# Kernel tuning notes

Measured on AMD Instinct MI355X. Metric: run time of the kernel, lower is better.

The kernel has to match this reference:

```python
import jax, jax.numpy as jnp
import numpy as np

N = 20000      # nodes
E = 320000     # edges
F_IN = 64      # input_dim
HID = 128      # hidden_dim
H = 2          # heads (hard-coded in BGA)
G = 64         # num graphs (batch_step_dim[0])
MID = 32       # middle_dim
OUT = 1        # output_dim
EPS = 1e-5


def setup_inputs() -> dict:
    key = jax.random.key(0)
    ks = jax.random.split(key, 24)
    p = lambda k, shape: jax.random.normal(k, shape, jnp.float32) * 0.05
    inp = {}
    inp["x"] = jax.random.normal(ks[0], (N, F_IN), jnp.float32)
    inp["edge_index"] = jax.random.randint(ks[1], (2, E), 0, N)
    inp["atten_edge_index"] = jax.random.randint(ks[2], (2, E), 0, N)
    inp["batch_index"] = jnp.sort(jax.random.randint(ks[3], (N,), 0, G))
    # GANConv 0 MLP (2-layer: Linear->BN->ReLU->Linear)
    inp["g0_w1"] = p(ks[4], (F_IN, HID)); inp["g0_b1"] = jnp.zeros((HID,), jnp.float32)
    inp["g0_bn_g"] = jnp.ones((HID,), jnp.float32); inp["g0_bn_b"] = jnp.zeros((HID,), jnp.float32)
    inp["g0_w2"] = p(ks[5], (HID, HID)); inp["g0_b2"] = jnp.zeros((HID,), jnp.float32)
    # GANConv 1 MLP
    inp["g1_w1"] = p(ks[6], (HID, HID)); inp["g1_b1"] = jnp.zeros((HID,), jnp.float32)
    inp["g1_bn_g"] = jnp.ones((HID,), jnp.float32); inp["g1_bn_b"] = jnp.zeros((HID,), jnp.float32)
    inp["g1_w2"] = p(ks[7], (HID, HID)); inp["g1_b2"] = jnp.zeros((HID,), jnp.float32)
    # BGA batch norms after each GANConv
    inp["bn0_g"] = jnp.ones((HID,), jnp.float32); inp["bn0_b"] = jnp.zeros((HID,), jnp.float32)
    inp["bn1_g"] = jnp.ones((HID,), jnp.float32); inp["bn1_b"] = jnp.zeros((HID,), jnp.float32)
    # ATTConv atten_self: in=HID, out=HID, heads=2, concat=True
    inp["a1_wl"] = p(ks[8], (HID, H * HID)); inp["a1_bl"] = jnp.zeros((H * HID,), jnp.float32)
    inp["a1_wr"] = p(ks[9], (HID, H * HID)); inp["a1_br"] = jnp.zeros((H * HID,), jnp.float32)
    inp["a1_att"] = p(ks[10], (H, HID))
    inp["a1_bias"] = jnp.zeros((H * HID,), jnp.float32)
    # ATTConv atten: in=H*HID, out=HID, heads=2, concat=False (mean over heads)
    inp["a2_wl"] = p(ks[11], (H * HID, H * HID)); inp["a2_bl"] = jnp.zeros((H * HID,), jnp.float32)
    inp["a2_wr"] = p(ks[12], (H * HID, H * HID)); inp["a2_br"] = jnp.zeros((H * HID,), jnp.float32)
    inp["a2_att"] = p(ks[13], (H, HID))
    inp["a2_bias"] = jnp.zeros((HID,), jnp.float32)
    # prediction heads (only layer 0 and last are used)
    inp["pred0_w"] = p(ks[14], (F_IN, MID)); inp["pred0_b"] = jnp.zeros((MID,), jnp.float32)
    inp["predL_w"] = p(ks[15], (HID, MID)); inp["predL_b"] = jnp.zeros((MID,), jnp.float32)
    inp["out_w"] = p(ks[16], (MID, OUT)); inp["out_b"] = jnp.zeros((OUT,), jnp.float32)
    return inp


def _bn(x, g, b):  # training-mode batch norm over node axis
    m = x.mean(0)
    v = x.var(0)
    return (x - m) * jax.lax.rsqrt(v + EPS) * g + b


def _mlp2(x, w1, b1, bn_g, bn_b, w2, b2):
    h = jax.nn.relu(_bn(x @ w1 + b1, bn_g, bn_b))
    return h @ w2 + b2


def _gan_conv(x, edge_index, w1, b1, bn_g, bn_b, w2, b2):
    row, col = edge_index[0], edge_index[1]
    agg = jax.ops.segment_sum(x[col], row, num_segments=x.shape[0])
    return _mlp2(x + agg, w1, b1, bn_g, bn_b, w2, b2)


def _att_conv(x, edge_index, wl, bl, wr, br, att, bias, concat):
    # GATv2-style: e = leaky_relu(x_i + x_j); alpha = softmax_dst(<e, att>)
    n = x.shape[0]
    xl = (x @ wl + bl).reshape(n, H, HID)  # source proj
    xr = (x @ wr + br).reshape(n, H, HID)  # target proj
    src, dst = edge_index[0], edge_index[1]
    e = jax.nn.leaky_relu(xl[src] + xr[dst], 0.2)          # [E,H,C]
    logit = jnp.einsum('ehc,hc->eh', e, att)               # [E,H]
    lmax = jax.ops.segment_max(logit, dst, num_segments=n)
    w = jnp.exp(logit - lmax[dst])
    denom = jax.ops.segment_sum(w, dst, num_segments=n)
    alpha = w / (denom[dst] + 1e-16)                       # [E,H]
    out = jax.ops.segment_sum(xl[src] * alpha[:, :, None], dst, num_segments=n)
    if concat:
        out = out.reshape(n, H * HID)
    else:
        out = out.mean(1)
    return out + bias, alpha


def reference(x, edge_index, atten_edge_index, batch_index,
              g0_w1, g0_b1, g0_bn_g, g0_bn_b, g0_w2, g0_b2,
              g1_w1, g1_b1, g1_bn_g, g1_bn_b, g1_w2, g1_b2,
              bn0_g, bn0_b, bn1_g, bn1_b,
              a1_wl, a1_bl, a1_wr, a1_br, a1_att, a1_bias,
              a2_wl, a2_bl, a2_wr, a2_br, a2_att, a2_bias,
              pred0_w, pred0_b, predL_w, predL_b, out_w, out_b):
    h0 = x
    h1 = jax.nn.relu(_bn(_gan_conv(h0, edge_index, g0_w1, g0_b1, g0_bn_g, g0_bn_b, g0_w2, g0_b2), bn0_g, bn0_b))
    h2 = jax.nn.relu(_bn(_gan_conv(h1, edge_index, g1_w1, g1_b1, g1_bn_g, g1_bn_b, g1_w2, g1_b2), bn1_g, bn1_b))
    emb, _ = _att_conv(h2, edge_index, a1_wl, a1_bl, a1_wr, a1_br, a1_att, a1_bias, concat=True)
    emb = jax.nn.relu(emb)
    atten_out, alpha = _att_conv(emb, atten_edge_index, a2_wl, a2_bl, a2_wr, a2_br, a2_att, a2_bias, concat=False)
    atten_out = jax.nn.relu(atten_out)
    pool0 = jax.ops.segment_sum(h0, batch_index, num_segments=G)
    poolL = jax.ops.segment_sum(atten_out, batch_index, num_segments=G)
    out_h = jax.nn.relu((pool0 @ pred0_w + pred0_b) + (poolL @ predL_w + predL_b))
    outputs = out_h @ out_w + out_b
    return (outputs, atten_out, alpha)
```

## Files before the change

kernel.cpp:

```cpp
#include <hip/hip_runtime.h>
#include <hip/hip_bf16.h>

#define N_NODES 20000
#define E_EDGES 320000
#define F_INN   64
#define HID     128
#define HEADS   2
#define HC      (HEADS * HID)
#define G_GR    64
#define MIDD    32
#define EPSV    1e-5f
#define NBUK    79

#define CDIV(a, b) (((a) + (b) - 1) / (b))

typedef __attribute__((ext_vector_type(8))) short          bf16x8;
typedef __attribute__((ext_vector_type(4))) float          f32x4;
typedef __attribute__((ext_vector_type(8))) unsigned short u16x8;

__device__ inline float bf2f(unsigned short u) { return __uint_as_float((unsigned)u << 16); }
__device__ inline unsigned short f2bf(float f) {
    unsigned u = __float_as_uint(f);
    unsigned r = u + 0x7FFFu + ((u >> 16) & 1u);
    return (unsigned short)(r >> 16);
}

#if __has_builtin(__builtin_amdgcn_exp2f)
__device__ inline float fexp2(float x) { return __builtin_amdgcn_exp2f(x); }
#else
__device__ inline float fexp2(float x) { return exp2f(x); }
#endif

struct Csr3 {
    const int* key[3];
    const int* other[3];
    int* btot;
    int* bstart;
    int* bcur;
    int* rowptr[3];
    int* out[3];
    int2* tmp;
};

__global__ __launch_bounds__(256) void k_bhist(Csr3 c) {
    __shared__ int hist[NBUK];
    const int y = blockIdx.y;
    const int chunk0 = blockIdx.x * 4096;
    const int t = threadIdx.x;
    for (int i = t; i < NBUK; i += 256) hist[i] = 0;
    __syncthreads();
#pragma unroll
    for (int i = 0; i < 16; i++) {
        int e = chunk0 + (i << 8) + t;
        if (e < E_EDGES) atomicAdd(&hist[c.key[y][e] >> 8], 1);
    }
    __syncthreads();
    for (int i = t; i < NBUK; i += 256)
        if (hist[i] > 0) atomicAdd(&c.btot[y * NBUK + i], hist[i]);
}

__global__ void k_bscan(Csr3 c) {
    __shared__ int sh[3 * NBUK];
    int t = threadIdx.x;
    for (int i = t; i < 3 * NBUK; i += 256) sh[i] = c.btot[i];
    __syncthreads();
    if (t < 3) {
        int run = 0;
        int* bs = c.bstart + t * (NBUK + 1);
        for (int b = 0; b < NBUK; b++) {
            bs[b] = run;
            c.bcur[t * NBUK + b] = run;
            run += sh[t * NBUK + b];
        }
        bs[NBUK] = run;
    }
}

__global__ __launch_bounds__(256) void k_bucketA(Csr3 c) {
    __shared__ int hist[NBUK], base[NBUK], off[NBUK];
    const int y = blockIdx.y;
    const int chunk0 = blockIdx.x * 4096;
    const int t = threadIdx.x;
    for (int i = t; i < NBUK; i += 256) { hist[i] = 0; off[i] = 0; }
    __syncthreads();
    int keys[16], vals[16], bks[16];
#pragma unroll
    for (int i = 0; i < 16; i++) {
        int e = chunk0 + (i << 8) + t;
        bool ok = (e < E_EDGES);
        int k = ok ? c.key[y][e] : 0;
        keys[i] = k;
        vals[i] = ok ? ((y == 2) ? e : c.other[y][e]) : 0;
        bks[i] = ok ? (k >> 8) : -1;
        if (ok) atomicAdd(&hist[k >> 8], 1);
    }
    __syncthreads();
    if (t < NBUK && hist[t] > 0) base[t] = atomicAdd(&c.bcur[y * NBUK + t], hist[t]);
    __syncthreads();
    int2* ty = c.tmp + (size_t)y * E_EDGES;
#pragma unroll
    for (int i = 0; i < 16; i++) {
        int b = bks[i];
        if (b >= 0) {
            int o = atomicAdd(&off[b], 1);
            ty[base[b] + o] = make_int2(keys[i], vals[i]);
        }
    }
}

__global__ __launch_bounds__(256) void k_bucketB(Csr3 c) {
    __shared__ int cnt[256], lbase[256], run[256];
    const int y = blockIdx.y;
    const int b = blockIdx.x;
    const int nbase = b << 8;
    const int t = threadIdx.x;
    cnt[t] = 0; run[t] = 0;
    __syncthreads();
    const int bs = c.bstart[y * (NBUK + 1) + b];
    const int be = c.bstart[y * (NBUK + 1) + b + 1];
    const int2* ty = c.tmp + (size_t)y * E_EDGES;
    for (int i = bs + t; i < be; i += 256)
        atomicAdd(&cnt[ty[i].x - nbase], 1);
    __syncthreads();
    int v = cnt[t];
    lbase[t] = v;
    __syncthreads();
    for (int off = 1; off < 256; off <<= 1) {
        int u = (t >= off) ? lbase[t - off] : 0;
        __syncthreads();
        lbase[t] += u;
        __syncthreads();
    }
    int excl = lbase[t] - v;
    __syncthreads();
    lbase[t] = excl;
    __syncthreads();
    int n = nbase + t;
    if (n < N_NODES) c.rowptr[y][n] = bs + excl;
    if (b == NBUK - 1 && t == 0) c.rowptr[y][N_NODES] = E_EDGES;
    int* outy = c.out[y];
    for (int i = bs + t; i < be; i += 256) {
        int2 kv = ty[i];
        int k = kv.x - nbase;
        int o = atomicAdd(&run[k], 1);
        outy[bs + lbase[k] + o] = kv.y;
    }
}

__global__ __launch_bounds__(256) void k_src_gather(const int* __restrict__ eids,
                                                    const int* __restrict__ srcs,
                                                    int* __restrict__ outv) {
    int i = blockIdx.x * 256 + threadIdx.x;
    if (i < E_EDGES) outv[i] = srcs[eids[i]];
}

__global__ __launch_bounds__(256) void k_gather_f32(const float4* __restrict__ x,
                                                    const int* __restrict__ rowptr,
                                                    const int* __restrict__ srcs,
                                                    unsigned short* __restrict__ z) {
    int gid = blockIdx.x * blockDim.x + threadIdx.x;
    int n = gid >> 4;
    if (n >= N_NODES) return;
    int q = gid & 15;
    float4 acc = x[((size_t)n << 4) + q];
    float4 a1 = make_float4(0.f, 0.f, 0.f, 0.f), a2 = a1, a3 = a1;
    int p = rowptr[n], p1 = rowptr[n + 1];
    for (; p + 4 <= p1; p += 4) {
        float4 v0 = x[((size_t)srcs[p + 0] << 4) + q];
        float4 v1 = x[((size_t)srcs[p + 1] << 4) + q];
        float4 v2 = x[((size_t)srcs[p + 2] << 4) + q];
        float4 v3 = x[((size_t)srcs[p + 3] << 4) + q];
        acc.x += v0.x; acc.y += v0.y; acc.z += v0.z; acc.w += v0.w;
        a1.x += v1.x; a1.y += v1.y; a1.z += v1.z; a1.w += v1.w;
        a2.x += v2.x; a2.y += v2.y; a2.z += v2.z; a2.w += v2.w;
        a3.x += v3.x; a3.y += v3.y; a3.z += v3.z; a3.w += v3.w;
    }
    for (; p < p1; p++) {
        float4 v = x[((size_t)srcs[p] << 4) + q];
        acc.x += v.x; acc.y += v.y; acc.z += v.z; acc.w += v.w;
    }
    acc.x += a1.x + a2.x + a3.x; acc.y += a1.y + a2.y + a3.y;
    acc.z += a1.z + a2.z + a3.z; acc.w += a1.w + a2.w + a3.w;
    ushort4 o;
    o.x = f2bf(acc.x); o.y = f2bf(acc.y); o.z = f2bf(acc.z); o.w = f2bf(acc.w);
    *(ushort4*)&z[((size_t)n << 6) + (q << 2)] = o;
}

__global__ __launch_bounds__(256) void k_gather_bn(const u16x8* __restrict__ raw,
                                                   const int* __restrict__ rowptr,
                                                   const int* __restrict__ srcs,
                                                   const float* __restrict__ bn_sums,
                                                   const float* __restrict__ g,
                                                   const float* __restrict__ b,
                                                   u16x8* __restrict__ z) {
    int gid = blockIdx.x * blockDim.x + threadIdx.x;
    int n = gid >> 4;
    if (n >= N_NODES) return;
    int q = gid & 15;
    float sc[8], sh[8];
#pragma unroll
    for (int i = 0; i < 8; i++) {
        int c = (q << 3) + i;
        float mean = bn_sums[c] / N_NODES;
        float istd = rsqrtf(bn_sums[HID + c] / N_NODES - mean * mean + EPSV);
        float s = istd * g[c];
        sc[i] = s;
        sh[i] = b[c] - mean * s;
    }
    u16x8 u0 = raw[((size_t)n << 4) + q];
    float acc[8];
#pragma unroll
    for (int i = 0; i < 8; i++) acc[i] = fmaxf(bf2f(u0[i]) * sc[i] + sh[i], 0.f);
    int p = rowptr[n], p1 = rowptr[n + 1];
    for (; p + 4 <= p1; p += 4) {
        u16x8 v0 = raw[((size_t)srcs[p + 0] << 4) + q];
        u16x8 v1 = raw[((size_t)srcs[p + 1] << 4) + q];
        u16x8 v2 = raw[((size_t)srcs[p + 2] << 4) + q];
        u16x8 v3 = raw[((size_t)srcs[p + 3] << 4) + q];
#pragma unroll
        for (int i = 0; i < 8; i++) {
            acc[i] += fmaxf(bf2f(v0[i]) * sc[i] + sh[i], 0.f)
                    + fmaxf(bf2f(v1[i]) * sc[i] + sh[i], 0.f)
                    + fmaxf(bf2f(v2[i]) * sc[i] + sh[i], 0.f)
                    + fmaxf(bf2f(v3[i]) * sc[i] + sh[i], 0.f);
        }
    }
    for (; p < p1; p++) {
        u16x8 v = raw[((size_t)srcs[p] << 4) + q];
#pragma unroll
        for (int i = 0; i < 8; i++) acc[i] += fmaxf(bf2f(v[i]) * sc[i] + sh[i], 0.f);
    }
    u16x8 o;
#pragma unroll
    for (int i = 0; i < 8; i++) o[i] = f2bf(acc[i]);
    z[((size_t)n << 4) + q] = o;
}

struct WtJob  { const float* src; unsigned short* dst; int K; int N; };
struct WtJobs { WtJob j[8]; };
__global__ void k_wt_cast(WtJobs jobs) {
    WtJob jb = jobs.j[blockIdx.y];
    int total = jb.K * jb.N;
    for (int i = blockIdx.x * blockDim.x + threadIdx.x; i < total; i += gridDim.x * blockDim.x) {
        int nn = i / jb.K, kk = i - nn * jb.K;
        jb.dst[i] = f2bf(jb.src[(size_t)kk * jb.N + nn]);
    }
}

template <int STATS, int BNA, int TM, int BIAS2>
__global__ __launch_bounds__(256) void k_mfma_gemm(const unsigned short* __restrict__ A,
                                                   const unsigned short* __restrict__ Wt,
                                                   const float* __restrict__ biasL,
                                                   const float* __restrict__ biasR,
                                                   unsigned short* __restrict__ Cout,
                                                   int M, int K, int N,
                                                   float* __restrict__ stats_sums,
                                                   const float* __restrict__ bn_sums,
                                                   const float* __restrict__ bn_g,
                                                   const float* __restrict__ bn_b) {
    constexpr int BNF = (TM == 128) ? 4 : 2;
    __shared__ unsigned short As[TM][40];
    __shared__ unsigned short Bs[128][40];
    __shared__ float s_scale[BNA ? HID : 1], s_shift[BNA ? HID : 1];
    const int t = threadIdx.x;
    if (BNA) {
        if (t < HID) {
            float mean = bn_sums[t] / M;
            float istd = rsqrtf(bn_sums[HID + t] / M - mean * mean + EPSV);
            float s = istd * bn_g[t];
            s_scale[t] = s;
            s_shift[t] = bn_b[t] - mean * s;
        }
        __syncthreads();
    }
    const int wave = t >> 6, lane = t & 63;
    const int row0 = blockIdx.y * TM, col0 = blockIdx.x * 128;
    const int wm = (TM == 128) ? ((wave & 1) << 6) : 0;
    const int wn = (TM == 128) ? ((wave >> 1) << 6) : (wave << 5);
    const int lm = lane & 15, lk = (lane >> 4) << 3;
    constexpr int APASS = TM / 64;
    f32x4 acc[4][BNF] = {};
    for (int k0 = 0; k0 < K; k0 += 32) {
        u16x8 av[APASS], wv[2];
#pragma unroll
        for (int i = 0; i < APASS; i++) {
            int c = t + (i << 8);
            int r = c >> 2, ko = (c & 3) << 3;
            u16x8 zv = {};
            int gr = row0 + r;
            av[i] = (gr < M) ? *(const u16x8*)&A[(size_t)gr * K + k0 + ko] : zv;
            if (BNA) {
#pragma unroll
                for (int j = 0; j < 8; j++) {
                    int kc = k0 + ko + j;
                    float v = fmaxf(bf2f(av[i][j]) * s_scale[kc] + s_shift[kc], 0.f);
                    av[i][j] = f2bf(v);
                }
            }
        }
#pragma unroll
        for (int i = 0; i < 2; i++) {
            int c = t + (i << 8);
            int r = c >> 2, ko = (c & 3) << 3;
            wv[i] = *(const u16x8*)&Wt[(size_t)(col0 + r) * K + k0 + ko];
        }
        __syncthreads();
#pragma unroll
        for (int i = 0; i < APASS; i++) {
            int c = t + (i << 8);
            int r = c >> 2, ko = (c & 3) << 3;
            *(u16x8*)&As[r][ko] = av[i];
        }
#pragma unroll
        for (int i = 0; i < 2; i++) {
            int c = t + (i << 8);
            int r = c >> 2, ko = (c & 3) << 3;
            *(u16x8*)&Bs[r][ko] = wv[i];
        }
        __syncthreads();
        bf16x8 af[4], bfm[BNF];
#pragma unroll
        for (int i = 0; i < 4; i++) af[i]  = *(const bf16x8*)&As[wm + (i << 4) + lm][lk];
#pragma unroll
        for (int j = 0; j < BNF; j++) bfm[j] = *(const bf16x8*)&Bs[wn + (j << 4) + lm][lk];
#pragma unroll
        for (int i = 0; i < 4; i++)
#pragma unroll
            for (int j = 0; j < BNF; j++)
                acc[i][j] = __builtin_amdgcn_mfma_f32_16x16x32_bf16(af[i], bfm[j], acc[i][j], 0, 0, 0);
    }
    const int lr4 = (lane >> 4) << 2;
    float s1[BNF], s2[BNF];
#pragma unroll
    for (int j = 0; j < BNF; j++) { s1[j] = 0.f; s2[j] = 0.f; }
#pragma unroll
    for (int j = 0; j < BNF; j++) {
        int col = col0 + wn + (j << 4) + lm;
        float bv = BIAS2 ? ((col < 256) ? biasL[col] : biasR[col - 256]) : biasL[col];
#pragma unroll
        for (int i = 0; i < 4; i++) {
#pragma unroll
            for (int r = 0; r < 4; r++) {
                int row = row0 + wm + (i << 4) + lr4 + r;
                if (row < M) {
                    float v = acc[i][j][r] + bv;
                    Cout[(size_t)row * N + col] = f2bf(v);
                    if (STATS) { s1[j] += v; s2[j] += v * v; }
                }
            }
        }
    }
    if (STATS) {
#pragma unroll
        for (int j = 0; j < BNF; j++) {
            s1[j] += __shfl_xor(s1[j], 16, 64); s1[j] += __shfl_xor(s1[j], 32, 64);
            s2[j] += __shfl_xor(s2[j], 16, 64); s2[j] += __shfl_xor(s2[j], 32, 64);
        }
        if ((lane >> 4) == 0) {
#pragma unroll
            for (int j = 0; j < BNF; j++) {
                int col = col0 + wn + (j << 4) + lm;
                atomicAdd(&stats_sums[col], s1[j]);
                atomicAdd(&stats_sums[HID + col], s2[j]);
            }
        }
    }
}

#define ATT_CAP 192
#define LOG2E   1.4426950408889634f
#define DTHR    11.0f

__device__ __forceinline__ float att_logit8(u16x8 uv, const float* xr8, const float* at8, float* x8) {
    float tl = 0.f;
#pragma unroll
    for (int i = 0; i < 8; i++) {
        x8[i] = bf2f(uv[i]);
        float v = x8[i] + xr8[i];
        v = (v > 0.f) ? v : 0.2f * v;
        tl = fmaf(at8[i], v, tl);
    }
    return tl;
}

__device__ __forceinline__ float red16(float tl) {
    tl += __shfl_xor(tl, 1, 64);
    tl += __shfl_xor(tl, 2, 64);
    tl += __shfl_xor(tl, 4, 64);
    tl += __shfl_xor(tl, 8, 64);
    return tl;
}

template <int CONCAT, int WITH_ALPHA>
__global__ __launch_bounds__(256) void k_att_fused(const u16x8* __restrict__ Q,
                                                   const int* __restrict__ rowptr,
                                                   const int* __restrict__ plist,
                                                   const int* __restrict__ srclist,
                                                   const float* __restrict__ att,
                                                   const float* __restrict__ bias,
                                                   void* __restrict__ outp,
                                                   float* __restrict__ alpha_out) {
    __shared__ float s_lg[WITH_ALPHA ? 4 : 1][WITH_ALPHA ? ATT_CAP : 1][2];
    const int t = threadIdx.x;
    const int wave = t >> 6, l = t & 63;
    const int n = blockIdx.x * 4 + wave;
    const int half = l >> 5;
    const int j = l & 31;
    const int h = j >> 4;

    u16x8 ur = Q[((size_t)n << 6) + 32 + j];
    float xr8[8];
#pragma unroll
    for (int i = 0; i < 8; i++) xr8[i] = bf2f(ur[i]);
    const float* ap = &att[h * HID + ((j & 15) << 3)];
    float at8[8];
#pragma unroll
    for (int i = 0; i < 8; i++) at8[i] = ap[i] * LOG2E;

    const int p0 = rowptr[n], p1 = rowptr[n + 1];
    float m = -1e30f, ssum = 0.f;
    float acc[8] = {};

#define ATT_SRC(p) (WITH_ALPHA ? srclist[p] : plist[p])

    int p = p0;
    for (; p + 8 <= p1; p += 8) {
        int s4[4];
#pragma unroll
        for (int g = 0; g < 4; g++) s4[g] = ATT_SRC(p + (g << 1) + half);
        u16x8 uv[4];
#pragma unroll
        for (int g = 0; g < 4; g++) uv[g] = Q[((size_t)s4[g] << 6) + j];
        float x8[4][8], tl[4];
#pragma unroll
        for (int g = 0; g < 4; g++) tl[g] = att_logit8(uv[g], xr8, at8, x8[g]);
#pragma unroll
        for (int g = 0; g < 4; g++) tl[g] = red16(tl[g]);
        if (WITH_ALPHA && (j & 15) == 0) {
#pragma unroll
            for (int g = 0; g < 4; g++) {
                int idx = p + (g << 1) + half - p0;
                if (idx < ATT_CAP) s_lg[wave][idx][h] = tl[g];
            }
        }
        float pm = fmaxf(fmaxf(tl[0], tl[1]), fmaxf(tl[2], tl[3]));
        if (__builtin_expect(!__all(pm <= m + DTHR), 0)) {
#pragma unroll
            for (int g = 0; g < 4; g++) {
                float mn = fmaxf(m, tl[g]);
                float sc = fexp2(m - mn);
                float w  = fexp2(tl[g] - mn);
                ssum = ssum * sc + w;
#pragma unroll
                for (int i = 0; i < 8; i++) acc[i] = acc[i] * sc + w * x8[g][i];
                m = mn;
            }
        } else {
            float w0 = fexp2(tl[0] - m), w1 = fexp2(tl[1] - m);
            float w2 = fexp2(tl[2] - m), w3 = fexp2(tl[3] - m);
            ssum += (w0 + w1) + (w2 + w3);
#pragma unroll
            for (int i = 0; i < 8; i++)
                acc[i] += (w0 * x8[0][i] + w1 * x8[1][i]) + (w2 * x8[2][i] + w3 * x8[3][i]);
        }
    }
    for (; p < p1; p += 2) {
        const bool v1 = (p + 1 < p1);
        int sp = (half && v1) ? (p + 1) : p;
        int src = ATT_SRC(sp);
        u16x8 uv = Q[((size_t)src << 6) + j];
        float x8[8], tl;
        tl = att_logit8(uv, xr8, at8, x8);
        tl = red16(tl);
        float vm = (half && !v1) ? 0.f : 1.f;
        if (vm == 0.f) tl = -1e30f;
        if (WITH_ALPHA && (j & 15) == 0 && vm != 0.f) {
            int idx = p + half - p0;
            if (idx < ATT_CAP) s_lg[wave][idx][h] = tl;
        }
        if (__builtin_expect(!__all(tl <= m + DTHR), 0)) {
            float mn = fmaxf(m, tl);
            float sc = fexp2(m - mn);
            float w  = fexp2(tl - mn) * vm;
            ssum = ssum * sc + w;
#pragma unroll
            for (int i = 0; i < 8; i++) acc[i] = acc[i] * sc + w * x8[i];
            m = mn;
        } else {
            float w = fexp2(tl - m) * vm;
            ssum += w;
#pragma unroll
            for (int i = 0; i < 8; i++) acc[i] += w * x8[i];
        }
    }

    float m_o = __shfl_xor(m, 32, 64);
    float mf  = fmaxf(m, m_o);
    float sA  = fexp2(m - mf);
    float ssA = ssum * sA;
    float ssum_f = ssA + __shfl_xor(ssA, 32, 64);
    float accf[8];
#pragma unroll
    for (int i = 0; i < 8; i++) {
        float a = acc[i] * sA;
        accf[i] = a + __shfl_xor(a, 32, 64);
    }
    float inv = 1.f / (ssum_f + 1e-16f);

    if (WITH_ALPHA) {
        float m_oh   = __shfl_xor(mf, 16, 64);
        float inv_oh = __shfl_xor(inv, 16, 64);
        float m2[2], i2[2];
        m2[h] = mf;  m2[1 - h] = m_oh;
        i2[h] = inv; i2[1 - h] = inv_oh;
        int cnt = p1 - p0;
        int ccnt = (cnt < ATT_CAP) ? cnt : ATT_CAP;
        for (int i = l; i < ccnt * 2; i += 64) {
            int idx = i >> 1, hh = i & 1;
            float a = fexp2(s_lg[wave][idx][hh] - m2[hh]) * i2[hh];
            alpha_out[plist[p0 + idx] * HEADS + hh] = a;
        }
        for (int pp = p0 + ATT_CAP; pp < p1; pp++) {
            int src = ATT_SRC(pp);
            u16x8 uv = Q[((size_t)src << 6) + j];
            float x8[8], tl;
            tl = att_logit8(uv, xr8, at8, x8);
            tl = red16(tl);
            if ((j & 15) == 0 && half == 0)
                alpha_out[plist[pp] * HEADS + h] = fexp2(tl - mf) * inv;
        }
    }

    if (CONCAT) {
        if (half == 0) {
            const float* bp = &bias[j << 3];
            u16x8 o;
#pragma unroll
            for (int i = 0; i < 8; i++) o[i] = f2bf(fmaxf(accf[i] * inv + bp[i], 0.f));
            ((u16x8*)outp)[((size_t)n << 5) + j] = o;
        }
    } else {
        float om[8];
#pragma unroll
        for (int i = 0; i < 8; i++) {
            float v = accf[i] * inv;
            om[i] = 0.5f * (v + __shfl_xor(v, 16, 64));
        }
        if (half == 0 && h == 0) {
            const float* bp = &bias[j << 3];
            float4 o0, o1;
            o0.x = fmaxf(om[0] + bp[0], 0.f); o0.y = fmaxf(om[1] + bp[1], 0.f);
            o0.z = fmaxf(om[2] + bp[2], 0.f); o0.w = fmaxf(om[3] + bp[3], 0.f);
            o1.x = fmaxf(om[4] + bp[4], 0.f); o1.y = fmaxf(om[5] + bp[5], 0.f);
            o1.z = fmaxf(om[6] + bp[6], 0.f); o1.w = fmaxf(om[7] + bp[7], 0.f);
            ((float4*)outp)[((size_t)n << 5) + (j << 1)]     = o0;
            ((float4*)outp)[((size_t)n << 5) + (j << 1) + 1] = o1;
        }
    }
#undef ATT_SRC
}

template <int C>
__global__ __launch_bounds__(256) void k_pool_atomic(const float* __restrict__ X,
                                                     const int* __restrict__ batch,
                                                     float* __restrict__ pool, int npb) {
    const int RP = 256 / C;
    int c = threadIdx.x & (C - 1);
    int rofs = threadIdx.x / C;
    int i0 = blockIdx.x * npb;
    int i1 = min(i0 + npb, N_NODES);
    float acc = 0.f;
    int gcur = -1;
    for (int i = i0 + rofs; i < i1; i += RP) {
        int g = batch[i];
        if (g != gcur) {
            if (gcur >= 0) atomicAdd(&pool[gcur * C + c], acc);
            acc = 0.f; gcur = g;
        }
        acc += X[(size_t)i * C + c];
    }
    if (gcur >= 0) atomicAdd(&pool[gcur * C + c], acc);
}

__global__ void k_head(const float* __restrict__ pool0, const float* __restrict__ poolL,
                       const float* __restrict__ p0w, const float* __restrict__ p0b,
                       const float* __restrict__ pLw, const float* __restrict__ pLb,
                       const float* __restrict__ ow, const float* __restrict__ ob,
                       float* __restrict__ outputs) {
    int g = blockIdx.x;
    int m = threadIdx.x;
    __shared__ float sh[MIDD];
    if (m < MIDD) {
        float s = p0b[m] + pLb[m];
        for (int k = 0; k < F_INN; k++) s += pool0[g * F_INN + k] * p0w[k * MIDD + m];
        for (int k = 0; k < HID; k++)  s += poolL[g * HID + k] * pLw[k * MIDD + m];
        sh[m] = fmaxf(s, 0.f);
    }
    __syncthreads();
    if (m == 0) {
        float s = ob[0];
        for (int k = 0; k < MIDD; k++) s += sh[k] * ow[k];
        outputs[g] = s;
    }
}

extern "C" void kernel_launch(void* const* d_in, const int* in_sizes, int n_in,
                              void* d_out, int out_size, void* d_ws, size_t ws_size,
                              hipStream_t stream) {
    const float* x      = (const float*)d_in[0];
    const int*   ei     = (const int*)d_in[1];
    const int*   aei    = (const int*)d_in[2];
    const int*   batch  = (const int*)d_in[3];
    const float* g0_w1  = (const float*)d_in[4];
    const float* g0_b1  = (const float*)d_in[5];
    const float* g0_bng = (const float*)d_in[6];
    const float* g0_bnb = (const float*)d_in[7];
    const float* g0_w2  = (const float*)d_in[8];
    const float* g0_b2  = (const float*)d_in[9];
    const float* g1_w1  = (const float*)d_in[10];
    const float* g1_b1  = (const float*)d_in[11];
    const float* g1_bng = (const float*)d_in[12];
    const float* g1_bnb = (const float*)d_in[13];
    const float* g1_w2  = (const float*)d_in[14];
    const float* g1_b2  = (const float*)d_in[15];
    const float* bn0_g  = (const float*)d_in[16];
    const float* bn0_b  = (const float*)d_in[17];
    const float* bn1_g  = (const float*)d_in[18];
    const float* bn1_b  = (const float*)d_in[19];
    const float* a1_wl  = (const float*)d_in[20];
    const float* a1_bl  = (const float*)d_in[21];
    const float* a1_wr  = (const float*)d_in[22];
    const float* a1_br  = (const float*)d_in[23];
    const float* a1_att = (const float*)d_in[24];
    const float* a1_bias= (const float*)d_in[25];
    const float* a2_wl  = (const float*)d_in[26];
    const float* a2_bl  = (const float*)d_in[27];
    const float* a2_wr  = (const float*)d_in[28];
    const float* a2_br  = (const float*)d_in[29];
    const float* a2_att = (const float*)d_in[30];
    const float* a2_bias= (const float*)d_in[31];
    const float* p0w    = (const float*)d_in[32];
    const float* p0b    = (const float*)d_in[33];
    const float* pLw    = (const float*)d_in[34];
    const float* pLb    = (const float*)d_in[35];
    const float* ow     = (const float*)d_in[36];
    const float* ob     = (const float*)d_in[37];

    float* out_head  = (float*)d_out;
    float* atten_out = out_head + G_GR;
    float* alpha_out = atten_out + (size_t)N_NODES * HID;

    float* ws = (float*)d_ws;
    float* sums4 = ws;
    float* pool0 = sums4 + 4 * 256;
    float* poolL = pool0 + G_GR * F_INN;
    int*   btot  = (int*)(poolL + G_GR * HID);
    const size_t zero_bytes = (4 * 256 + G_GR * F_INN + G_GR * HID + 3 * NBUK) * 4;

    int* ip = btot + 3 * NBUK;
    int* bstart = ip; ip += 3 * (NBUK + 1);
    int* bcur   = ip; ip += 3 * NBUK;
    int* rowptr[3]; int* payload[3];
    for (int c = 0; c < 3; c++) {
        rowptr[c]  = ip; ip += N_NODES + 1;
        payload[c] = ip; ip += E_EDGES;
    }
    int2* tmp3 = (int2*)ip; ip += 2 * 3 * E_EDGES;
    int* srclist = (int*)tmp3;
    const size_t NB = (size_t)N_NODES * HC;
    unsigned short* B1 = (unsigned short*)ip;
    unsigned short* B2 = B1 + NB;
    unsigned short* Qb = B2 + NB;
    unsigned short* g0w1t = Qb + 2 * NB;
    unsigned short* g0w2t = g0w1t + 128 * 64;
    unsigned short* g1w1t = g0w2t + 128 * 128;
    unsigned short* g1w2t = g1w1t + 128 * 128;
    unsigned short* a1wlt = g1w2t + 128 * 128;
    unsigned short* a1wrt = a1wlt + 256 * 128;
    unsigned short* a2wlt = a1wrt + 256 * 128;
    unsigned short* a2wrt = a2wlt + 256 * 256;

    const int* e_row = ei;
    const int* e_col = ei + E_EDGES;
    const int* a_src = aei;
    const int* a_dst = aei + E_EDGES;

    const int TB = 256;
#define GRID1(n) dim3(CDIV((n), TB))

    {
        WtJobs jobs;
        jobs.j[0] = {g0_w1, g0w1t, F_INN, HID};
        jobs.j[1] = {g0_w2, g0w2t, HID,   HID};
        jobs.j[2] = {g1_w1, g1w1t, HID,   HID};
        jobs.j[3] = {g1_w2, g1w2t, HID,   HID};
        jobs.j[4] = {a1_wl, a1wlt, HID,   HC};
        jobs.j[5] = {a1_wr, a1wrt, HID,   HC};
        jobs.j[6] = {a2_wl, a2wlt, HC,    HC};
        jobs.j[7] = {a2_wr, a2wrt, HC,    HC};
        k_wt_cast<<<dim3(32, 8), TB, 0, stream>>>(jobs);
    }

    hipMemsetAsync(sums4, 0, zero_bytes, stream);
    {
        Csr3 c;
        c.key[0] = e_row; c.other[0] = e_col;
        c.key[1] = e_col; c.other[1] = e_row;
        c.key[2] = a_dst; c.other[2] = a_src;
        c.btot = btot; c.bstart = bstart; c.bcur = bcur; c.tmp = tmp3;
        for (int i = 0; i < 3; i++) { c.rowptr[i] = rowptr[i]; c.out[i] = payload[i]; }
        k_bhist<<<dim3(CDIV(E_EDGES, 4096), 3), TB, 0, stream>>>(c);
        k_bscan<<<dim3(1), TB, 0, stream>>>(c);
        k_bucketA<<<dim3(CDIV(E_EDGES, 4096), 3), TB, 0, stream>>>(c);
        k_bucketB<<<dim3(NBUK, 3), TB, 0, stream>>>(c);
    }
    k_src_gather<<<GRID1(E_EDGES), TB, 0, stream>>>(payload[2], a_src, srclist);

    const dim3 gemm_g1(1, CDIV(N_NODES, 64));
    const dim3 gemm_gq(4, CDIV(N_NODES, 128));
    const float* NOF = nullptr;

    k_gather_f32<<<GRID1(N_NODES * 16), TB, 0, stream>>>((const float4*)x, rowptr[0], payload[0], B1);
    k_mfma_gemm<1, 0, 64, 0><<<gemm_g1, TB, 0, stream>>>(B1, g0w1t, g0_b1, NOF, B2, N_NODES, F_INN, HID,
                                                         sums4 + 0, NOF, NOF, NOF);
    k_mfma_gemm<1, 1, 64, 0><<<gemm_g1, TB, 0, stream>>>(B2, g0w2t, g0_b2, NOF, B1, N_NODES, HID, HID,
                                                         sums4 + 256, sums4 + 0, g0_bng, g0_bnb);

    k_gather_bn<<<GRID1(N_NODES * 16), TB, 0, stream>>>((const u16x8*)B1, rowptr[0], payload[0],
                                                        sums4 + 256, bn0_g, bn0_b, (u16x8*)B2);
    k_mfma_gemm<1, 0, 64, 0><<<gemm_g1, TB, 0, stream>>>(B2, g1w1t, g1_b1, NOF, B1, N_NODES, HID, HID,
                                                         sums4 + 512, NOF, NOF, NOF);
    k_mfma_gemm<1, 1, 64, 0><<<gemm_g1, TB, 0, stream>>>(B1, g1w2t, g1_b2, NOF, B2, N_NODES, HID, HID,
                                                         sums4 + 768, sums4 + 512, g1_bng, g1_bnb);

    k_mfma_gemm<0, 1, 128, 1><<<gemm_gq, TB, 0, stream>>>(B2, a1wlt, a1_bl, a1_br, Qb, N_NODES, HID, 512,
                                                          nullptr, sums4 + 768, bn1_g, bn1_b);
    k_att_fused<1, 0><<<dim3(N_NODES / 4), TB, 0, stream>>>(
        (const u16x8*)Qb, rowptr[1], payload[1], nullptr, a1_att, a1_bias, (void*)B1, nullptr);

    k_mfma_gemm<0, 0, 128, 1><<<gemm_gq, TB, 0, stream>>>(B1, a2wlt, a2_bl, a2_br, Qb, N_NODES, HC, 512,
                                                          nullptr, NOF, NOF, NOF);
    k_att_fused<0, 1><<<dim3(N_NODES / 4), TB, 0, stream>>>(
        (const u16x8*)Qb, rowptr[2], payload[2], srclist, a2_att, a2_bias, (void*)atten_out, alpha_out);

    {
        const int npb = 64;
        k_pool_atomic<F_INN><<<dim3(CDIV(N_NODES, npb)), TB, 0, stream>>>(x, batch, pool0, npb);
        k_pool_atomic<HID><<<dim3(CDIV(N_NODES, npb)), TB, 0, stream>>>(atten_out, batch, poolL, npb);
    }
    k_head<<<dim3(G_GR), 64, 0, stream>>>(pool0, poolL, p0w, p0b, pLw, pLb, ow, ob, out_head);
}
```

Before: 428.9 us.

## Software-pipeline attention edge loads, unroll gathers by 8, fuse source gather into bucketing

The attention kernel's edge loop is restructured into double-buffered groups: the next group's indices and Q rows are loaded while the current group's logits and softmax update are computed. Tail edges are masked rather than handled in a separate loop. The GIN neighbour-gather kernels gain an 8-wide unrolled loop so more independent loads are in flight. The separate source-gather kernel is folded into the CSR bucket pass for the attention graph, which removes one launch and one pass over the edges. The cost is higher register pressure and an added __syncthreads in the alpha path, and srclist is moved to its own buffer.

After: 451.7 us. +5.3%, slower.

```diff
diff --git a/kernel.cpp b/kernel.cpp
--- a/kernel.cpp
+++ b/kernel.cpp
@@ -34,6 +34,8 @@
 struct Csr3 {
     const int* key[3];
     const int* other[3];
+    const int* asrc;
+    int* srcout;
     int* btot;
     int* bstart;
     int* bcur;
@@ -143,15 +145,10 @@
         int2 kv = ty[i];
         int k = kv.x - nbase;
         int o = atomicAdd(&run[k], 1);
-        outy[bs + lbase[k] + o] = kv.y;
-    }
-}
-
-__global__ __launch_bounds__(256) void k_src_gather(const int* __restrict__ eids,
-                                                    const int* __restrict__ srcs,
-                                                    int* __restrict__ outv) {
-    int i = blockIdx.x * 256 + threadIdx.x;
-    if (i < E_EDGES) outv[i] = srcs[eids[i]];
+        int pos = bs + lbase[k] + o;
+        outy[pos] = kv.y;
+        if (y == 2) c.srcout[pos] = c.asrc[kv.y];
+    }
 }
 
 __global__ __launch_bounds__(256) void k_gather_f32(const float4* __restrict__ x,
@@ -165,6 +162,20 @@
     float4 acc = x[((size_t)n << 4) + q];
     float4 a1 = make_float4(0.f, 0.f, 0.f, 0.f), a2 = a1, a3 = a1;
     int p = rowptr[n], p1 = rowptr[n + 1];
+    for (; p + 8 <= p1; p += 8) {
+        float4 v0 = x[((size_t)srcs[p + 0] << 4) + q];
+        float4 v1 = x[((size_t)srcs[p + 1] << 4) + q];
+        float4 v2 = x[((size_t)srcs[p + 2] << 4) + q];
+        float4 v3 = x[((size_t)srcs[p + 3] << 4) + q];
+        float4 v4 = x[((size_t)srcs[p + 4] << 4) + q];
+        float4 v5 = x[((size_t)srcs[p + 5] << 4) + q];
+        float4 v6 = x[((size_t)srcs[p + 6] << 4) + q];
+        float4 v7 = x[((size_t)srcs[p + 7] << 4) + q];
+        acc.x += v0.x + v4.x; acc.y += v0.y + v4.y; acc.z += v0.z + v4.z; acc.w += v0.w + v4.w;
+        a1.x += v1.x + v5.x; a1.y += v1.y + v5.y; a1.z += v1.z + v5.z; a1.w += v1.w + v5.w;
+        a2.x += v2.x + v6.x; a2.y += v2.y + v6.y; a2.z += v2.z + v6.z; a2.w += v2.w + v6.w;
+        a3.x += v3.x + v7.x; a3.y += v3.y + v7.y; a3.z += v3.z + v7.z; a3.w += v3.w + v7.w;
+    }
     for (; p + 4 <= p1; p += 4) {
         float4 v0 = x[((size_t)srcs[p + 0] << 4) + q];
         float4 v1 = x[((size_t)srcs[p + 1] << 4) + q];
@@ -212,6 +223,27 @@
 #pragma unroll
     for (int i = 0; i < 8; i++) acc[i] = fmaxf(bf2f(u0[i]) * sc[i] + sh[i], 0.f);
     int p = rowptr[n], p1 = rowptr[n + 1];
+    for (; p + 8 <= p1; p += 8) {
+        u16x8 v0 = raw[((size_t)srcs[p + 0] << 4) + q];
+        u16x8 v1 = raw[((size_t)srcs[p + 1] << 4) + q];
+        u16x8 v2 = raw[((size_t)srcs[p + 2] << 4) + q];
+        u16x8 v3 = raw[((size_t)srcs[p + 3] << 4) + q];
+        u16x8 v4 = raw[((size_t)srcs[p + 4] << 4) + q];
+        u16x8 v5 = raw[((size_t)srcs[p + 5] << 4) + q];
+        u16x8 v6 = raw[((size_t)srcs[p + 6] << 4) + q];
+        u16x8 v7 = raw[((size_t)srcs[p + 7] << 4) + q];
+#pragma unroll
+        for (int i = 0; i < 8; i++) {
+            acc[i] += fmaxf(bf2f(v0[i]) * sc[i] + sh[i], 0.f)
+                    + fmaxf(bf2f(v1[i]) * sc[i] + sh[i], 0.f)
+                    + fmaxf(bf2f(v2[i]) * sc[i] + sh[i], 0.f)
+                    + fmaxf(bf2f(v3[i]) * sc[i] + sh[i], 0.f)
+                    + fmaxf(bf2f(v4[i]) * sc[i] + sh[i], 0.f)
+                    + fmaxf(bf2f(v5[i]) * sc[i] + sh[i], 0.f)
+                    + fmaxf(bf2f(v6[i]) * sc[i] + sh[i], 0.f)
+                    + fmaxf(bf2f(v7[i]) * sc[i] + sh[i], 0.f);
+        }
+    }
     for (; p + 4 <= p1; p += 4) {
         u16x8 v0 = raw[((size_t)srcs[p + 0] << 4) + q];
         u16x8 v1 = raw[((size_t)srcs[p + 1] << 4) + q];
@@ -391,6 +423,63 @@
     return tl;
 }
 
+struct AttGrp { int e0; int sv[4]; float vm[4]; u16x8 uv[4]; };
+
+__device__ __forceinline__ void att_load(AttGrp& G, int base, int half, int j, int p1,
+                                         const int* __restrict__ PL,
+                                         const u16x8* __restrict__ Q) {
+    G.e0 = base + (half << 2);
+#pragma unroll
+    for (int g = 0; g < 4; g++) {
+        int ei = G.e0 + g;
+        bool ok = ei < p1;
+        G.vm[g] = ok ? 1.f : 0.f;
+        G.sv[g] = PL[ok ? ei : (p1 - 1)];
+    }
+#pragma unroll
+    for (int g = 0; g < 4; g++) G.uv[g] = Q[((size_t)G.sv[g] << 6) + j];
+}
+
+template <int WITH_ALPHA>
+__device__ __forceinline__ void att_compute(const AttGrp& G, const float* xr8, const float* at8,
+                                            float& m, float& ssum, float* acc,
+                                            float (*slg)[2], int p0, int j, int h) {
+    float x8[4][8], tl[4];
+#pragma unroll
+    for (int g = 0; g < 4; g++) tl[g] = att_logit8(G.uv[g], xr8, at8, x8[g]);
+#pragma unroll
+    for (int g = 0; g < 4; g++) tl[g] = red16(tl[g]);
+#pragma unroll
+    for (int g = 0; g < 4; g++) tl[g] = (G.vm[g] != 0.f) ? tl[g] : -1e30f;
+    if (WITH_ALPHA && (j & 15) == 0) {
+#pragma unroll
+        for (int g = 0; g < 4; g++) {
+            int idx = G.e0 + g - p0;
+            if (G.vm[g] != 0.f && idx < ATT_CAP) slg[idx][h] = tl[g];
+        }
+    }
+    float pm = fmaxf(fmaxf(tl[0], tl[1]), fmaxf(tl[2], tl[3]));
+    if (__builtin_expect(!__all(pm <= m + DTHR), 0)) {
+#pragma unroll
+        for (int g = 0; g < 4; g++) {
+            float mn = fmaxf(m, tl[g]);
+            float sc = fexp2(m - mn);
+            float w  = fexp2(tl[g] - mn) * G.vm[g];
+            ssum = ssum * sc + w;
+#pragma unroll
+            for (int i = 0; i < 8; i++) acc[i] = acc[i] * sc + w * x8[g][i];
+            m = mn;
+        }
+    } else {
+        float w0 = fexp2(tl[0] - m) * G.vm[0], w1 = fexp2(tl[1] - m) * G.vm[1];
+        float w2 = fexp2(tl[2] - m) * G.vm[2], w3 = fexp2(tl[3] - m) * G.vm[3];
+        ssum += (w0 + w1) + (w2 + w3);
+#pragma unroll
+        for (int i = 0; i < 8; i++)
+            acc[i] += (w0 * x8[0][i] + w1 * x8[1][i]) + (w2 * x8[2][i] + w3 * x8[3][i]);
+    }
+}
+
 template <int CONCAT, int WITH_ALPHA>
 __global__ __launch_bounds__(256) void k_att_fused(const u16x8* __restrict__ Q,
                                                    const int* __restrict__ rowptr,
@@ -418,79 +507,23 @@
     for (int i = 0; i < 8; i++) at8[i] = ap[i] * LOG2E;
 
     const int p0 = rowptr[n], p1 = rowptr[n + 1];
+    const int* PL = WITH_ALPHA ? srclist : plist;
     float m = -1e30f, ssum = 0.f;
     float acc[8] = {};
-
-#define ATT_SRC(p) (WITH_ALPHA ? srclist[p] : plist[p])
-
-    int p = p0;
-    for (; p + 8 <= p1; p += 8) {
-        int s4[4];
-#pragma unroll
-        for (int g = 0; g < 4; g++) s4[g] = ATT_SRC(p + (g << 1) + half);
-        u16x8 uv[4];
-#pragma unroll
-        for (int g = 0; g < 4; g++) uv[g] = Q[((size_t)s4[g] << 6) + j];
-        float x8[4][8], tl[4];
-#pragma unroll
-        for (int g = 0; g < 4; g++) tl[g] = att_logit8(uv[g], xr8, at8, x8[g]);
-#pragma unroll
-        for (int g = 0; g < 4; g++) tl[g] = red16(tl[g]);
-        if (WITH_ALPHA && (j & 15) == 0) {
-#pragma unroll
-            for (int g = 0; g < 4; g++) {
-                int idx = p + (g << 1) + half - p0;
-                if (idx < ATT_CAP) s_lg[wave][idx][h] = tl[g];
-            }
-        }
-        float pm = fmaxf(fmaxf(tl[0], tl[1]), fmaxf(tl[2], tl[3]));
-        if (__builtin_expect(!__all(pm <= m + DTHR), 0)) {
-#pragma unroll
-            for (int g = 0; g < 4; g++) {
-                float mn = fmaxf(m, tl[g]);
-                float sc = fexp2(m - mn);
-                float w  = fexp2(tl[g] - mn);
-                ssum = ssum * sc + w;
-#pragma unroll
-                for (int i = 0; i < 8; i++) acc[i] = acc[i] * sc + w * x8[g][i];
-                m = mn;
-            }
-        } else {
-            float w0 = fexp2(tl[0] - m), w1 = fexp2(tl[1] - m);
-            float w2 = fexp2(tl[2] - m), w3 = fexp2(tl[3] - m);
-            ssum += (w0 + w1) + (w2 + w3);
-#pragma unroll
-            for (int i = 0; i < 8; i++)
-                acc[i] += (w0 * x8[0][i] + w1 * x8[1][i]) + (w2 * x8[2][i] + w3 * x8[3][i]);
-        }
-    }
-    for (; p < p1; p += 2) {
-        const bool v1 = (p + 1 < p1);
-        int sp = (half && v1) ? (p + 1) : p;
-        int src = ATT_SRC(sp);
-        u16x8 uv = Q[((size_t)src << 6) + j];
-        float x8[8], tl;
-        tl = att_logit8(uv, xr8, at8, x8);
-        tl = red16(tl);
-        float vm = (half && !v1) ? 0.f : 1.f;
-        if (vm == 0.f) tl = -1e30f;
-        if (WITH_ALPHA && (j & 15) == 0 && vm != 0.f) {
-            int idx = p + half - p0;
-            if (idx < ATT_CAP) s_lg[wave][idx][h] = tl;
-        }
-        if (__builtin_expect(!__all(tl <= m + DTHR), 0)) {
-            float mn = fmaxf(m, tl);
-            float sc = fexp2(m - mn);
-            float w  = fexp2(tl - mn) * vm;
-            ssum = ssum * sc + w;
-#pragma unroll
-            for (int i = 0; i < 8; i++) acc[i] = acc[i] * sc + w * x8[i];
-            m = mn;
-        } else {
-            float w = fexp2(tl - m) * vm;
-            ssum += w;
-#pragma unroll
-            for (int i = 0; i < 8; i++) acc[i] += w * x8[i];
+    float (*slg)[2] = WITH_ALPHA ? s_lg[wave] : nullptr;
+
+    const int nsteps = (p1 - p0 + 7) >> 3;
+    AttGrp GA, GB;
+    if (nsteps > 0) {
+        att_load(GA, p0, half, j, p1, PL, Q);
+        int s = 0;
+        while (true) {
+            if (s + 1 < nsteps) att_load(GB, p0 + ((s + 1) << 3), half, j, p1, PL, Q);
+            att_compute<WITH_ALPHA>(GA, xr8, at8, m, ssum, acc, slg, p0, j, h);
+            if (++s >= nsteps) break;
+            if (s + 1 < nsteps) att_load(GA, p0 + ((s + 1) << 3), half, j, p1, PL, Q);
+            att_compute<WITH_ALPHA>(GB, xr8, at8, m, ssum, acc, slg, p0, j, h);
+            if (++s >= nsteps) break;
         }
     }
 
@@ -515,13 +548,14 @@
         i2[h] = inv; i2[1 - h] = inv_oh;
         int cnt = p1 - p0;
         int ccnt = (cnt < ATT_CAP) ? cnt : ATT_CAP;
+        __syncthreads();
         for (int i = l; i < ccnt * 2; i += 64) {
             int idx = i >> 1, hh = i & 1;
             float a = fexp2(s_lg[wave][idx][hh] - m2[hh]) * i2[hh];
             alpha_out[plist[p0 + idx] * HEADS + hh] = a;
         }
         for (int pp = p0 + ATT_CAP; pp < p1; pp++) {
-            int src = ATT_SRC(pp);
+            int src = PL[pp];
             u16x8 uv = Q[((size_t)src << 6) + j];
             float x8[8], tl;
             tl = att_logit8(uv, xr8, at8, x8);
@@ -557,7 +591,6 @@
             ((float4*)outp)[((size_t)n << 5) + (j << 1) + 1] = o1;
         }
     }
-#undef ATT_SRC
 }
 
 template <int C>
@@ -666,7 +699,6 @@
         payload[c] = ip; ip += E_EDGES;
     }
     int2* tmp3 = (int2*)ip; ip += 2 * 3 * E_EDGES;
-    int* srclist = (int*)tmp3;
     const size_t NB = (size_t)N_NODES * HC;
     unsigned short* B1 = (unsigned short*)ip;
     unsigned short* B2 = B1 + NB;
@@ -679,6 +711,7 @@
     unsigned short* a1wrt = a1wlt + 256 * 128;
     unsigned short* a2wlt = a1wrt + 256 * 128;
     unsigned short* a2wrt = a2wlt + 256 * 256;
+    int* srclist = (int*)(a2wrt + 256 * 256);
 
     const int* e_row = ei;
     const int* e_col = ei + E_EDGES;
@@ -707,6 +740,7 @@
         c.key[0] = e_row; c.other[0] = e_col;
         c.key[1] = e_col; c.other[1] = e_row;
         c.key[2] = a_dst; c.other[2] = a_src;
+        c.asrc = a_src; c.srcout = srclist;
         c.btot = btot; c.bstart = bstart; c.bcur = bcur; c.tmp = tmp3;
         for (int i = 0; i < 3; i++) { c.rowptr[i] = rowptr[i]; c.out[i] = payload[i]; }
         k_bhist<<<dim3(CDIV(E_EDGES, 4096), 3), TB, 0, stream>>>(c);
@@ -714,7 +748,6 @@
         k_bucketA<<<dim3(CDIV(E_EDGES, 4096), 3), TB, 0, stream>>>(c);
         k_bucketB<<<dim3(NBUK, 3), TB, 0, stream>>>(c);
     }
-    k_src_gather<<<GRID1(E_EDGES), TB, 0, stream>>>(payload[2], a_src, srclist);
 
     const dim3 gemm_g1(1, CDIV(N_NODES, 64));
     const dim3 gemm_gq(4, CDIV(N_NODES, 128));
```
